# Optimization experiments

Hardware: AMD Instinct MI355X
Metric: run time of the kernel (lower is better)

Reference implementation:

```python
import jax, jax.numpy as jnp
from jax import lax
import numpy as np

K = 5  # length_inter_tile
EPS = 0.01


def _conv(x, w, b):
    y = lax.conv_general_dilated(x, w, (1, 1), ((1, 1), (1, 1)),
                                 dimension_numbers=('NCHW', 'OIHW', 'NCHW'))
    return y + b[None, :, None, None]


def _leaky(x):
    return jnp.where(x >= 0, x, 0.01 * x)


def _unfold(x, k=K):
    # torch F.unfold(x, k, padding=k//2): (b,c,h,w) -> (b, c*k*k, h*w), channel-major ordering
    b, c, h, w = x.shape
    p = k // 2
    xp = jnp.pad(x, ((0, 0), (0, 0), (p, p), (p, p)))
    pat = jnp.stack([xp[:, :, i:i + h, j:j + w] for i in range(k) for j in range(k)], axis=2)
    return pat.reshape(b, c * k * k, h * w)


def _fold(x, c, h, w, k=K):
    # torch F.fold: (b, c*k*k, h*w) -> (b, c, h, w) with overlap-add, padding=k//2
    b = x.shape[0]
    p = k // 2
    xr = x.reshape(b, c, k, k, h, w)
    out = jnp.zeros((b, c, h + 2 * p, w + 2 * p), x.dtype)
    for i in range(k):
        for j in range(k):
            out = out.at[:, :, i:i + h, j:j + w].add(xr[:, :, i, j])
    return out[:, :, p:p + h, p:p + w]


def _mmn(x, axes):
    mn = jnp.min(x, axis=axes, keepdims=True)
    mx = jnp.max(x, axis=axes, keepdims=True)
    return (x - mn) / (mx - mn + 0.001)


def setup_inputs() -> dict:
    key = jax.random.key(0)
    ks = jax.random.split(key, 8)
    b, t, ch_in, h, w = 1, 16, 10, 24, 24
    t_de, ch_de = 16, 12
    sc = 0.02
    return {
        'x': jax.random.normal(ks[0], (b, t, ch_in, h, w), jnp.float32),
        'design': jax.random.uniform(ks[1], (b, t_de, ch_de, h, w), jnp.float32),
        'gt': jax.random.uniform(ks[2], (b, t_de, 3, h, w), jnp.float32),
        'w1': jax.random.normal(ks[3], (1024, 160, 3, 3), jnp.float32) * sc,
        'b1': jnp.zeros((1024,), jnp.float32),
        'w2': jax.random.normal(ks[4], (1024, 1024, 3, 3), jnp.float32) * sc,
        'b2': jnp.zeros((1024,), jnp.float32),
        'w3': jax.random.normal(ks[5], (1024, 1024, 3, 3), jnp.float32) * sc,
        'b3': jnp.zeros((1024,), jnp.float32),
        'wf': jax.random.normal(ks[6], (6400, 1024, 3, 3), jnp.float32) * sc,
        'bf': jnp.zeros((6400,), jnp.float32),
    }


def _forward(x, design, gt, w1, b1, w2, b2, w3, b3, wf, bf):
    b, t, ch_in, h, w = x.shape
    t_de, ch_de = design.shape[1], design.shape[2]
    hw = h * w
    N = K * K  # num_inter

    # unfold design: (b, t_de*ch_de*N, hw) -> (b*hw, N, t_de, ch_de)
    d = _unfold(design.reshape(b, t_de * ch_de, h, w))
    d = d.transpose(0, 2, 1).reshape(b * hw, t_de * ch_de, N)
    d = d.transpose(0, 2, 1).reshape(b * hw, N, t_de, ch_de)

    # norm in each prediction window (per channel-group, per sample)
    d = jnp.concatenate([
        d[..., 0:1],
        _mmn(d[..., 1:4], (1, 2, 3)),
        _mmn(d[..., 4:5], (1, 2)),
        _mmn(d[..., 5:8], (1, 2, 3)),
        _mmn(d[..., 8:], (1, 2)),  # each grid channel independently
    ], axis=-1)

    M = b * hw * N
    domain = d.reshape(M, t_de, ch_de)
    X = d[:, :, :t, :].reshape(M, t, ch_de)

    # feature network (n_layers=4 -> 3 leaky convs) + weight head
    f = _leaky(_conv(x.reshape(b, t * ch_in, h, w), w1, b1))
    f = _leaky(_conv(f, w2, b2))
    f = _leaky(_conv(f, w3, b3))
    Wt = jnp.tanh(_conv(f, wf, bf))  # (b, N*t*t, h, w)
    Wm = Wt.reshape(b, N, t, t, h, w).transpose(0, 4, 5, 1, 2, 3).reshape(M, t, t)
    Wm = jnp.einsum('nij,nkj->nik', Wm, Wm) + jnp.eye(t, dtype=Wm.dtype)

    XTW = jnp.einsum('ntc,ntu->ncu', X, Wm)          # (M, ch_de, t)
    XTWX = jnp.einsum('nct,ntd->ncd', XTW, X)        # (M, ch_de, ch_de)
    A = XTWX.reshape(b * hw, N, ch_de, ch_de).sum(1) + EPS * jnp.eye(ch_de, dtype=XTWX.dtype)

    # reference for loss (unfolded)
    ref = _unfold(gt.reshape(b, t_de * 3, h, w))
    ref = ref.transpose(0, 2, 1).reshape(b * hw, t_de * 3, N)
    ref = ref.transpose(0, 2, 1).reshape(M, t_de, 3)

    outs, folded = [], []
    for ch in range(3):
        Y = _unfold(x[:, :, ch])                      # (b, t*N, hw)
        Y = Y.transpose(0, 2, 1).reshape(b * hw, t, N)
        Y = Y.transpose(0, 2, 1).reshape(M, t, 1)
        XTWY = jnp.einsum('nct,nto->nco', XTW, Y)
        Bv = XTWY.reshape(b * hw, N, ch_de, 1).sum(1)
        para = jnp.linalg.solve(A, Bv)                # (b*hw, ch_de, 1)
        para_r = jnp.broadcast_to(para[:, None], (b * hw, N, ch_de, 1)).reshape(M, ch_de, 1)
        o = jnp.einsum('ntc,nco->nto', domain, para_r)  # (M, t_de, 1)
        outs.append(o[..., 0])
        # overlap-add fold of per-window predictions
        oc = o.reshape(b, hw, N, t_de).transpose(0, 3, 2, 1).reshape(b, t_de * N, hw)
        num = _fold(oc, t_de, h, w)
        den = _fold(jnp.ones_like(oc), t_de, h, w)
        folded.append(num / den)

    out_for_loss = jnp.stack(outs, axis=-1)           # (M, t_de, 3)
    out = jnp.stack(folded, axis=2)                   # (b, t_de, 3, h, w)
    loss = jnp.mean(jnp.abs(out_for_loss - ref))      # L1 stand-in for loss_for_stit_v1
    return out, loss


def reference(x, design, gt, w1, b1, w2, b2, w3, b3, wf, bf):
    return _forward(x, design, gt, w1, b1, w2, b2, w3, b3, wf, bf)
```

## Files before the change

### kernel.cpp

```cpp
#include <hip/hip_runtime.h>
#include <math.h>


typedef __attribute__((ext_vector_type(8))) short sh8;
typedef __attribute__((ext_vector_type(4))) float f32x4;

#define OFF_PART 0UL
#define OFF_X2T  58982400UL
#define OFF_WTT  58982400UL
#define OFF_ACT  80216064UL
#define OFF_OB   82575360UL
#define OFF_LP   85340160UL


__device__ inline void glds16(const void* gsrc, void* ldst) {
    __builtin_amdgcn_global_load_lds((const __attribute__((address_space(1))) void*)gsrc,
                                     (__attribute__((address_space(3))) void*)ldst, 16, 0, 0);
}

__global__ __launch_bounds__(256) void im2col_kernel(const float* __restrict__ act,
                                                     char* __restrict__ x2t, int nrows) {
    int row = blockIdx.x * 256 + threadIdx.x;
    if (row >= nrows) return;
    int kc = row / 576, px = row % 576;
    int y = px / 24, x = px % 24;
    int k0 = kc * 32;
    int ic = k0 / 9;
    int tap = k0 - ic * 9;
    sh8 hv[4], lv[4];
#pragma unroll
    for (int e = 0; e < 32; ++e) {
        int dy = tap / 3, dx = tap - dy * 3;
        int yy = y + dy - 1, xx = x + dx - 1;
        float v = (yy >= 0 && yy < 24 && xx >= 0 && xx < 24)
                      ? act[ic * 576 + yy * 24 + xx] : 0.0f;
        unsigned u = __builtin_bit_cast(unsigned, v);
        hv[e / 8][e % 8] = (short)(u >> 16);
        float fh = __builtin_bit_cast(float, u & 0xFFFF0000u);
        lv[e / 8][e % 8] = (short)(__builtin_bit_cast(unsigned, v - fh) >> 16);
        if (++tap == 9) { tap = 0; ++ic; }
    }
    int pg = px >> 4, l15 = px & 15;
    char* dst = x2t + (long)kc * 73728 + pg * 2048 + l15 * 16;
#pragma unroll
    for (int q = 0; q < 4; ++q) {
        *(sh8*)(dst + q * 256) = hv[q];
        *(sh8*)(dst + 1024 + q * 256) = lv[q];
    }
}

__global__ void finalize_kernel(const float* __restrict__ part,
                                const float* __restrict__ bias,
                                float* __restrict__ act, int total, int nsplit) {
    int idx = blockIdx.x * 256 + threadIdx.x;
    if (idx >= total) return;
    float s = 0.0f;
    for (int k = 0; k < nsplit; k++) s += part[(long)k * total + idx];
    s += bias[idx / 576];
    act[idx] = s >= 0.0f ? s : 0.01f * s;
}

template<int SWZ>
__global__ __launch_bounds__(256, 4)
void conv_mfma8_kernel(const char* __restrict__ x2t,
                       const float* __restrict__ wgt,
                       float* __restrict__ part,
                       int K, int cps, int cout) {
    __shared__ __align__(1024) char sB[18432];
    __shared__ __align__(1024) char sA[16384];

    const int tid = threadIdx.x;
    const int lane = tid & 63;
    const int w = tid >> 6;
    const int q = lane >> 4, ln15 = lane & 15;
    const int lane16 = lane * 16;

    int ocb, pxq, s;
    if (SWZ) {
        int g = blockIdx.x;
        int p = (g & 7) * 100 + (g >> 3);
        ocb = p / 16;
        int rem = p % 16;
        s = rem >> 2; pxq = rem & 3;
    } else {
        ocb = blockIdx.x; pxq = blockIdx.y; s = blockIdx.z;
    }
    const int c0 = s * cps;

    const int st_oc = tid >> 1, st_h = tid & 1;
    const float* wrow = wgt + (long)(ocb * 128 + st_oc) * K + st_h * 16;
    const int wslot0 = (((st_h * 2 + 0) + (st_oc >> 1)) & 3) << 4;
    const int wslot1 = (((st_h * 2 + 1) + (st_oc >> 1)) & 3) << 4;

    int aoff[2];
#pragma unroll
    for (int ot = 0; ot < 2; ++ot) {
        int oc = w * 32 + ot * 16 + ln15;
        aoff[ot] = oc * 64 + (((q + (oc >> 1)) & 3) << 4);
    }

    f32x4 acc[2][9];
#pragma unroll
    for (int a = 0; a < 2; ++a)
#pragma unroll
        for (int j = 0; j < 9; ++j) acc[a][j] = f32x4{0.f, 0.f, 0.f, 0.f};

#pragma unroll 1
    for (int t = 0; t < cps; ++t) {
        const int cc = c0 + t;
        __syncthreads();
        const char* bsrc = x2t + (long)cc * 73728 + pxq * 18432;
        for (int u = w; u < 18; u += 4)
            glds16(bsrc + u * 1024 + lane16, sB + u * 1024);
        {
            const float* p = wrow + (long)cc * 32;
            float4 a0 = *(const float4*)(p);
            float4 a1 = *(const float4*)(p + 4);
            float4 a2 = *(const float4*)(p + 8);
            float4 a3 = *(const float4*)(p + 12);
            float av[16] = {a0.x, a0.y, a0.z, a0.w, a1.x, a1.y, a1.z, a1.w,
                            a2.x, a2.y, a2.z, a2.w, a3.x, a3.y, a3.z, a3.w};
            sh8 h8[2], l8[2];
#pragma unroll
            for (int e = 0; e < 16; ++e) {
                unsigned u = __builtin_bit_cast(unsigned, av[e]);
                h8[e / 8][e % 8] = (short)(u >> 16);
                float fh = __builtin_bit_cast(float, u & 0xFFFF0000u);
                l8[e / 8][e % 8] = (short)(__builtin_bit_cast(unsigned, av[e] - fh) >> 16);
            }
            char* hb = sA + st_oc * 64;
            *(sh8*)(hb + wslot0) = h8[0];
            *(sh8*)(hb + wslot1) = h8[1];
            *(sh8*)(hb + 8192 + wslot0) = l8[0];
            *(sh8*)(hb + 8192 + wslot1) = l8[1];
        }
        asm volatile("s_waitcnt vmcnt(0)" ::: "memory");
        __syncthreads();

        sh8 ah[2], al[2];
#pragma unroll
        for (int ot = 0; ot < 2; ++ot) {
            ah[ot] = *(const sh8*)(sA + aoff[ot]);
            al[ot] = *(const sh8*)(sA + 8192 + aoff[ot]);
        }
#pragma unroll
        for (int j = 0; j < 9; ++j) {
            sh8 bh = *(const sh8*)(sB + j * 2048 + lane16);
            sh8 bl = *(const sh8*)(sB + j * 2048 + 1024 + lane16);
#pragma unroll
            for (int ot = 0; ot < 2; ++ot) {
                acc[ot][j] = __builtin_amdgcn_mfma_f32_16x16x32_bf16(ah[ot], bh, acc[ot][j], 0, 0, 0);
                acc[ot][j] = __builtin_amdgcn_mfma_f32_16x16x32_bf16(al[ot], bh, acc[ot][j], 0, 0, 0);
                acc[ot][j] = __builtin_amdgcn_mfma_f32_16x16x32_bf16(ah[ot], bl, acc[ot][j], 0, 0, 0);
            }
        }
    }
#pragma unroll
    for (int ot = 0; ot < 2; ++ot) {
        int oc0 = ocb * 128 + w * 32 + ot * 16 + q * 4;
#pragma unroll
        for (int j = 0; j < 9; ++j) {
            int px = pxq * 144 + j * 16 + ln15;
#pragma unroll
            for (int vr = 0; vr < 4; ++vr)
                part[((long)s * cout + oc0 + vr) * 576 + px] = acc[ot][j][vr];
        }
    }
}

__global__ __launch_bounds__(256) void tanh_tr_kernel(const float* __restrict__ part,
                                                      const float* __restrict__ bias,
                                                      float* __restrict__ wtT, int nsplit) {
    __shared__ float tile[64][65];
    int oc0 = blockIdx.x * 64, p0 = blockIdx.y * 64;
    int tx = threadIdx.x, ty = threadIdx.y;
#pragma unroll
    for (int k = 0; k < 16; k++) {
        int row = ty + k * 4;
        float s = 0.f;
        for (int sp = 0; sp < nsplit; ++sp)
            s += part[((long)sp * 6400 + oc0 + row) * 576 + p0 + tx];
        tile[row][tx] = tanhf(s + bias[oc0 + row]);
    }
    __syncthreads();
#pragma unroll
    for (int k = 0; k < 16; k++) {
        int rr = ty + k * 4;
        wtT[(long)(p0 + rr) * 6400 + oc0 + tx] = tile[tx][rr];
    }
}

__global__ __launch_bounds__(256) void stagec_kernel(const float* __restrict__ design,
                                                     const float* __restrict__ wtT,
                                                     const float* __restrict__ xin,
                                                     const float* __restrict__ gt,
                                                     float* __restrict__ ob,
                                                     float* __restrict__ lp) {
    int p = blockIdx.x;
    int py = p / 24, px = p % 24;
    int tid = threadIdx.x;
    int lane = tid & 63, wv = tid >> 6;
    __shared__ float sX[4800];
    __shared__ float sW[6400];
    __shared__ float sY[1200];
    __shared__ float sP[192];
    __shared__ float sXTW[192];
    __shared__ float sA[144];
    __shared__ float sB[36];
    __shared__ double dM[180];
    __shared__ float spara[36];
    __shared__ float sred[256];
    __shared__ float sMnW[28], sMxW[28], sMn[7], sMx[7];

    for (int e = tid; e < 4800; e += 256) {
        int n = e / 192, r = e % 192, td = r / 12, cd = r % 12;
        int yy = py + n / 5 - 2, xx = px + n % 5 - 2;
        sX[e] = (yy >= 0 && yy < 24 && xx >= 0 && xx < 24)
                    ? design[(td * 12 + cd) * 576 + yy * 24 + xx] : 0.0f;
    }
    for (int e = tid; e < 6400; e += 256) sW[e] = wtT[(long)p * 6400 + e];
    for (int e = tid; e < 1200; e += 256) {
        int n = e / 48, t = (e % 48) / 3, ch = e % 3;
        int yy = py + n / 5 - 2, xx = px + n % 5 - 2;
        sY[e] = (yy >= 0 && yy < 24 && xx >= 0 && xx < 24)
                    ? xin[(t * 10 + ch) * 576 + yy * 24 + xx] : 0.0f;
    }
    if (tid < 144) sA[tid] = 0.0f;
    if (tid < 36) sB[tid] = 0.0f;
    __syncthreads();

    {
        float mn[7], mx[7];
#pragma unroll
        for (int g = 0; g < 7; g++) { mn[g] = 1e30f; mx[g] = -1e30f; }
        for (int e = tid; e < 4800; e += 256) {
            int cd = e % 12;
            if (cd >= 1) {
                int g = (cd <= 3) ? 0 : (cd == 4) ? 1 : (cd <= 7) ? 2 : 3 + (cd - 8);
                float v = sX[e];
                mn[g] = fminf(mn[g], v);
                mx[g] = fmaxf(mx[g], v);
            }
        }
#pragma unroll
        for (int s2 = 32; s2 >= 1; s2 >>= 1)
#pragma unroll
            for (int g = 0; g < 7; g++) {
                mn[g] = fminf(mn[g], __shfl_xor(mn[g], s2));
                mx[g] = fmaxf(mx[g], __shfl_xor(mx[g], s2));
            }
        if (lane == 0)
#pragma unroll
            for (int g = 0; g < 7; g++) { sMnW[wv * 7 + g] = mn[g]; sMxW[wv * 7 + g] = mx[g]; }
    }
    __syncthreads();
    if (tid < 7) {
        float a = fminf(fminf(sMnW[tid], sMnW[7 + tid]), fminf(sMnW[14 + tid], sMnW[21 + tid]));
        float b = fmaxf(fmaxf(sMxW[tid], sMxW[7 + tid]), fmaxf(sMxW[14 + tid], sMxW[21 + tid]));
        sMn[tid] = a; sMx[tid] = b;
    }
    __syncthreads();
    for (int e = tid; e < 4800; e += 256) {
        int cd = e % 12;
        if (cd >= 1) {
            int g = (cd <= 3) ? 0 : (cd == 4) ? 1 : (cd <= 7) ? 2 : 3 + (cd - 8);
            sX[e] = (sX[e] - sMn[g]) / (sMx[g] - sMn[g] + 0.001f);
        }
    }
    __syncthreads();

    for (int n = 0; n < 25; n++) {
        const float* X = sX + n * 192;
        const float* W = sW + n * 256;
        if (tid < 192) {
            int c = tid >> 4, j = tid & 15;
            float s = 0.0f;
#pragma unroll
            for (int t = 0; t < 16; t++) s = fmaf(X[t * 12 + c], W[t * 16 + j], s);
            sP[tid] = s;
        }
        __syncthreads();
        if (tid < 192) {
            int c = tid >> 4, u = tid & 15;
            float s = X[u * 12 + c];
#pragma unroll
            for (int j = 0; j < 16; j++) s = fmaf(sP[c * 16 + j], W[u * 16 + j], s);
            sXTW[tid] = s;
        }
        __syncthreads();
        if (tid < 144) {
            int c = tid / 12, d2 = tid % 12;
            float s = 0.0f;
#pragma unroll
            for (int t = 0; t < 16; t++) s = fmaf(sXTW[c * 16 + t], X[t * 12 + d2], s);
            sA[tid] += s;
        } else if (tid < 180) {
            int e = tid - 144;
            int c = e / 3, ch = e % 3;
            float s = 0.0f;
#pragma unroll
            for (int t = 0; t < 16; t++) s = fmaf(sXTW[c * 16 + t], sY[n * 48 + t * 3 + ch], s);
            sB[e] += s;
        }
        __syncthreads();
    }

    if (tid < 144) dM[(tid / 12) * 15 + (tid % 12)] = (double)sA[tid] + ((tid % 13 == 0) ? 0.01 : 0.0);
    if (tid < 36) dM[(tid / 3) * 15 + 12 + (tid % 3)] = (double)sB[tid];
    __syncthreads();
    {
        int rr = (tid < 180) ? tid / 15 : 11;
        int c2 = (tid < 180) ? tid % 15 : 14;
#pragma unroll 1
        for (int k = 0; k < 12; ++k) {
            double pinv = 1.0 / dM[k * 15 + k];
            double fkc = dM[k * 15 + c2] * pinv;
            double frk = dM[rr * 15 + k];
            double cur = dM[rr * 15 + c2];
            __syncthreads();
            if (tid < 180) dM[rr * 15 + c2] = (rr == k) ? fkc : fma(-frk, fkc, cur);
            __syncthreads();
        }
    }
    if (tid < 36) spara[tid] = (float)dM[(tid / 3) * 15 + 12 + (tid % 3)];
    __syncthreads();

    float lsum = 0.0f;
    for (int e = tid; e < 1200; e += 256) {
        int n = e / 48, td = (e % 48) / 3, ch = e % 3;
        float s = 0.0f;
#pragma unroll
        for (int c = 0; c < 12; c++) s = fmaf(sX[n * 192 + td * 12 + c], spara[c * 3 + ch], s);
        ob[((long)(p * 25 + n)) * 48 + td * 3 + ch] = s;
        int yy = py + n / 5 - 2, xx = px + n % 5 - 2;
        float rv = (yy >= 0 && yy < 24 && xx >= 0 && xx < 24)
                       ? gt[(td * 3 + ch) * 576 + yy * 24 + xx] : 0.0f;
        lsum += fabsf(s - rv);
    }
    sred[tid] = lsum;
    __syncthreads();
    for (int s = 128; s >= 1; s >>= 1) {
        if (tid < s) sred[tid] += sred[tid + s];
        __syncthreads();
    }
    if (tid == 0) lp[p] = sred[0];
}

__global__ void fold_kernel(const float* __restrict__ ob, float* __restrict__ out) {
    int idx = blockIdx.x * 256 + threadIdx.x;
    if (idx >= 27648) return;
    int td = idx / 1728;
    int rem = idx % 1728;
    int ch = rem / 576;
    int p = rem % 576;
    int y = p / 24, x = p % 24;
    float num = 0.0f;
    int den = 0;
    for (int i = 0; i < 5; i++) {
        int yy = y + 2 - i;
        if (yy < 0 || yy >= 24) continue;
        for (int j = 0; j < 5; j++) {
            int xx = x + 2 - j;
            if (xx < 0 || xx >= 24) continue;
            num += ob[((long)((yy * 24 + xx) * 25 + i * 5 + j)) * 48 + td * 3 + ch];
            den++;
        }
    }
    out[idx] = num / (float)den;
}

__global__ __launch_bounds__(64) void loss_kernel(const float* __restrict__ lp,
                                                  float* __restrict__ out) {
    int t = threadIdx.x;
    float s = 0.0f;
    for (int e = t; e < 576; e += 64) s += lp[e];
#pragma unroll
    for (int d = 32; d >= 1; d >>= 1) s += __shfl_xor(s, d);
    if (t == 0) out[27648] = s / 691200.0f;
}

extern "C" void kernel_launch(void* const* d_in, const int* in_sizes, int n_in,
                              void* d_out, int out_size, void* d_ws, size_t ws_size,
                              hipStream_t stream) {
    const float* x      = (const float*)d_in[0];
    const float* design = (const float*)d_in[1];
    const float* gt     = (const float*)d_in[2];
    const float* w1     = (const float*)d_in[3];
    const float* b1     = (const float*)d_in[4];
    const float* w2     = (const float*)d_in[5];
    const float* b2     = (const float*)d_in[6];
    const float* w3     = (const float*)d_in[7];
    const float* b3     = (const float*)d_in[8];
    const float* wf     = (const float*)d_in[9];
    const float* bf     = (const float*)d_in[10];
    float* out = (float*)d_out;
    char* wsb  = (char*)d_ws;

    float* part = (float*)(wsb + OFF_PART);
    char*  x2t  = wsb + OFF_X2T;
    float* wtT  = (float*)(wsb + OFF_WTT);
    float* act  = (float*)(wsb + OFF_ACT);
    float* ob   = (float*)(wsb + OFF_OB);
    float* lp   = (float*)(wsb + OFF_LP);

    im2col_kernel<<<102, 256, 0, stream>>>(x, x2t, 45 * 576);
    conv_mfma8_kernel<0><<<dim3(8, 4, 15), 256, 0, stream>>>(x2t, w1, part, 1440, 3, 1024);
    finalize_kernel<<<2304, 256, 0, stream>>>(part, b1, act, 589824, 15);
    im2col_kernel<<<648, 256, 0, stream>>>(act, x2t, 288 * 576);
    conv_mfma8_kernel<0><<<dim3(8, 4, 16), 256, 0, stream>>>(x2t, w2, part, 9216, 18, 1024);
    finalize_kernel<<<2304, 256, 0, stream>>>(part, b2, act, 589824, 16);
    im2col_kernel<<<648, 256, 0, stream>>>(act, x2t, 288 * 576);
    conv_mfma8_kernel<0><<<dim3(8, 4, 16), 256, 0, stream>>>(x2t, w3, part, 9216, 18, 1024);
    finalize_kernel<<<2304, 256, 0, stream>>>(part, b3, act, 589824, 16);
    im2col_kernel<<<648, 256, 0, stream>>>(act, x2t, 288 * 576);
    conv_mfma8_kernel<1><<<800, 256, 0, stream>>>(x2t, wf, part, 9216, 72, 6400);
    tanh_tr_kernel<<<dim3(100, 9), dim3(64, 4), 0, stream>>>(part, bf, wtT, 4);

    stagec_kernel<<<576, 256, 0, stream>>>(design, wtT, x, gt, ob, lp);
    fold_kernel<<<108, 256, 0, stream>>>(ob, out);
    loss_kernel<<<1, 64, 0, stream>>>(lp, out);
}
```

Measured before the change: 506.6 us.

## Replace LDS-staged conv GEMM with register double-buffered direct loads

The conv MFMA kernel no longer stages A and B tiles through shared memory with barriers. Each wave now loads its B fragments and weight rows straight from global memory into registers and prefetches the next K-chunk while the MFMAs for the current one run. The final conv layer drops from 4 to 2 split-K partitions (400 blocks), which shrinks the partial-sum buffer, and the workspace offsets move to match. The trade-off is higher register pressure (launch bounds go from 4 to 2 blocks per CU), redundant global loads of B across waves that LDS used to share, and less parallelism in the final layer.

```diff
diff --git a/kernel.cpp b/kernel.cpp
--- a/kernel.cpp
+++ b/kernel.cpp
@@ -6,17 +6,12 @@
 typedef __attribute__((ext_vector_type(4))) float f32x4;
 
 #define OFF_PART 0UL
-#define OFF_X2T  58982400UL
-#define OFF_WTT  58982400UL
-#define OFF_ACT  80216064UL
-#define OFF_OB   82575360UL
-#define OFF_LP   85340160UL
-
-
-__device__ inline void glds16(const void* gsrc, void* ldst) {
-    __builtin_amdgcn_global_load_lds((const __attribute__((address_space(1))) void*)gsrc,
-                                     (__attribute__((address_space(3))) void*)ldst, 16, 0, 0);
-}
+#define OFF_X2T  37748736UL
+#define OFF_WTT  37748736UL
+#define OFF_ACT  58982400UL
+#define OFF_OB   61341696UL
+#define OFF_LP   64106496UL
+
 
 __global__ __launch_bounds__(256) void im2col_kernel(const float* __restrict__ act,
                                                      char* __restrict__ x2t, int nrows) {
@@ -60,15 +55,23 @@
     act[idx] = s >= 0.0f ? s : 0.01f * s;
 }
 
+__device__ inline void cvt_split8(const float4& a0, const float4& a1, sh8& h8, sh8& l8) {
+    float av[8] = {a0.x, a0.y, a0.z, a0.w, a1.x, a1.y, a1.z, a1.w};
+#pragma unroll
+    for (int e = 0; e < 8; ++e) {
+        unsigned u = __builtin_bit_cast(unsigned, av[e]);
+        h8[e] = (short)(u >> 16);
+        float fh = __builtin_bit_cast(float, u & 0xFFFF0000u);
+        l8[e] = (short)(__builtin_bit_cast(unsigned, av[e] - fh) >> 16);
+    }
+}
+
 template<int SWZ>
-__global__ __launch_bounds__(256, 4)
-void conv_mfma8_kernel(const char* __restrict__ x2t,
+__global__ __launch_bounds__(256, 2)
+void conv_mfma9_kernel(const char* __restrict__ x2t,
                        const float* __restrict__ wgt,
                        float* __restrict__ part,
                        int K, int cps, int cout) {
-    __shared__ __align__(1024) char sB[18432];
-    __shared__ __align__(1024) char sA[16384];
-
     const int tid = threadIdx.x;
     const int lane = tid & 63;
     const int w = tid >> 6;
@@ -78,81 +81,75 @@
     int ocb, pxq, s;
     if (SWZ) {
         int g = blockIdx.x;
-        int p = (g & 7) * 100 + (g >> 3);
-        ocb = p / 16;
-        int rem = p % 16;
+        int p = (g & 7) * 50 + (g >> 3);
+        ocb = p >> 3;
+        int rem = p & 7;
         s = rem >> 2; pxq = rem & 3;
     } else {
         ocb = blockIdx.x; pxq = blockIdx.y; s = blockIdx.z;
     }
     const int c0 = s * cps;
 
-    const int st_oc = tid >> 1, st_h = tid & 1;
-    const float* wrow = wgt + (long)(ocb * 128 + st_oc) * K + st_h * 16;
-    const int wslot0 = (((st_h * 2 + 0) + (st_oc >> 1)) & 3) << 4;
-    const int wslot1 = (((st_h * 2 + 1) + (st_oc >> 1)) & 3) << 4;
-
-    int aoff[2];
-#pragma unroll
-    for (int ot = 0; ot < 2; ++ot) {
-        int oc = w * 32 + ot * 16 + ln15;
-        aoff[ot] = oc * 64 + (((q + (oc >> 1)) & 3) << 4);
-    }
+    const float* arow0 = wgt + (long)(ocb * 128 + w * 32 + ln15) * K + q * 8;
+    const float* arow1 = arow0 + (long)16 * K;
+    const char* bbase = x2t + (long)pxq * 18432;
 
     f32x4 acc[2][9];
 #pragma unroll
     for (int a = 0; a < 2; ++a)
 #pragma unroll
         for (int j = 0; j < 9; ++j) acc[a][j] = f32x4{0.f, 0.f, 0.f, 0.f};
+
+    sh8 bh[9], bl[9];
+    {
+        const char* bc = bbase + (long)c0 * 73728;
+#pragma unroll
+        for (int j = 0; j < 9; ++j) {
+            bh[j] = *(const sh8*)(bc + j * 2048 + lane16);
+            bl[j] = *(const sh8*)(bc + j * 2048 + 1024 + lane16);
+        }
+    }
+    sh8 ah[2], al[2];
+    float4 an[4];
+    {
+        const float* p0 = arow0 + (long)c0 * 32;
+        const float* p1 = arow1 + (long)c0 * 32;
+        float4 t0 = *(const float4*)(p0), t1 = *(const float4*)(p0 + 4);
+        float4 t2 = *(const float4*)(p1), t3 = *(const float4*)(p1 + 4);
+        cvt_split8(t0, t1, ah[0], al[0]);
+        cvt_split8(t2, t3, ah[1], al[1]);
+        const int c1 = (cps > 1) ? c0 + 1 : c0;
+        const float* n0 = arow0 + (long)c1 * 32;
+        const float* n1 = arow1 + (long)c1 * 32;
+        an[0] = *(const float4*)(n0); an[1] = *(const float4*)(n0 + 4);
+        an[2] = *(const float4*)(n1); an[3] = *(const float4*)(n1 + 4);
+    }
 
 #pragma unroll 1
     for (int t = 0; t < cps; ++t) {
-        const int cc = c0 + t;
-        __syncthreads();
-        const char* bsrc = x2t + (long)cc * 73728 + pxq * 18432;
-        for (int u = w; u < 18; u += 4)
-            glds16(bsrc + u * 1024 + lane16, sB + u * 1024);
-        {
-            const float* p = wrow + (long)cc * 32;
-            float4 a0 = *(const float4*)(p);
-            float4 a1 = *(const float4*)(p + 4);
-            float4 a2 = *(const float4*)(p + 8);
-            float4 a3 = *(const float4*)(p + 12);
-            float av[16] = {a0.x, a0.y, a0.z, a0.w, a1.x, a1.y, a1.z, a1.w,
-                            a2.x, a2.y, a2.z, a2.w, a3.x, a3.y, a3.z, a3.w};
-            sh8 h8[2], l8[2];
-#pragma unroll
-            for (int e = 0; e < 16; ++e) {
-                unsigned u = __builtin_bit_cast(unsigned, av[e]);
-                h8[e / 8][e % 8] = (short)(u >> 16);
-                float fh = __builtin_bit_cast(float, u & 0xFFFF0000u);
-                l8[e / 8][e % 8] = (short)(__builtin_bit_cast(unsigned, av[e] - fh) >> 16);
-            }
-            char* hb = sA + st_oc * 64;
-            *(sh8*)(hb + wslot0) = h8[0];
-            *(sh8*)(hb + wslot1) = h8[1];
-            *(sh8*)(hb + 8192 + wslot0) = l8[0];
-            *(sh8*)(hb + 8192 + wslot1) = l8[1];
-        }
-        asm volatile("s_waitcnt vmcnt(0)" ::: "memory");
-        __syncthreads();
-
-        sh8 ah[2], al[2];
-#pragma unroll
-        for (int ot = 0; ot < 2; ++ot) {
-            ah[ot] = *(const sh8*)(sA + aoff[ot]);
-            al[ot] = *(const sh8*)(sA + 8192 + aoff[ot]);
-        }
+        const int cn = (t + 1 < cps) ? (c0 + t + 1) : (c0 + cps - 1);
+        const char* bnext = bbase + (long)cn * 73728;
 #pragma unroll
         for (int j = 0; j < 9; ++j) {
-            sh8 bh = *(const sh8*)(sB + j * 2048 + lane16);
-            sh8 bl = *(const sh8*)(sB + j * 2048 + 1024 + lane16);
-#pragma unroll
-            for (int ot = 0; ot < 2; ++ot) {
-                acc[ot][j] = __builtin_amdgcn_mfma_f32_16x16x32_bf16(ah[ot], bh, acc[ot][j], 0, 0, 0);
-                acc[ot][j] = __builtin_amdgcn_mfma_f32_16x16x32_bf16(al[ot], bh, acc[ot][j], 0, 0, 0);
-                acc[ot][j] = __builtin_amdgcn_mfma_f32_16x16x32_bf16(ah[ot], bl, acc[ot][j], 0, 0, 0);
-            }
+            sh8 bhj = bh[j];
+            sh8 blj = bl[j];
+            acc[0][j] = __builtin_amdgcn_mfma_f32_16x16x32_bf16(ah[0], bhj, acc[0][j], 0, 0, 0);
+            acc[1][j] = __builtin_amdgcn_mfma_f32_16x16x32_bf16(ah[1], bhj, acc[1][j], 0, 0, 0);
+            acc[0][j] = __builtin_amdgcn_mfma_f32_16x16x32_bf16(al[0], bhj, acc[0][j], 0, 0, 0);
+            acc[1][j] = __builtin_amdgcn_mfma_f32_16x16x32_bf16(al[1], bhj, acc[1][j], 0, 0, 0);
+            acc[0][j] = __builtin_amdgcn_mfma_f32_16x16x32_bf16(ah[0], blj, acc[0][j], 0, 0, 0);
+            acc[1][j] = __builtin_amdgcn_mfma_f32_16x16x32_bf16(ah[1], blj, acc[1][j], 0, 0, 0);
+            bh[j] = *(const sh8*)(bnext + j * 2048 + lane16);
+            bl[j] = *(const sh8*)(bnext + j * 2048 + 1024 + lane16);
+        }
+        if (t + 1 < cps) {
+            cvt_split8(an[0], an[1], ah[0], al[0]);
+            cvt_split8(an[2], an[3], ah[1], al[1]);
+            const int c2 = (t + 2 < cps) ? (c0 + t + 2) : (c0 + cps - 1);
+            const float* n0 = arow0 + (long)c2 * 32;
+            const float* n1 = arow1 + (long)c2 * 32;
+            an[0] = *(const float4*)(n0); an[1] = *(const float4*)(n0 + 4);
+            an[2] = *(const float4*)(n1); an[3] = *(const float4*)(n1 + 4);
         }
     }
 #pragma unroll
@@ -255,9 +252,8 @@
     }
     __syncthreads();
     if (tid < 7) {
-        float a = fminf(fminf(sMnW[tid], sMnW[7 + tid]), fminf(sMnW[14 + tid], sMnW[21 + tid]));
-        float b = fmaxf(fmaxf(sMxW[tid], sMxW[7 + tid]), fmaxf(sMxW[14 + tid], sMxW[21 + tid]));
-        sMn[tid] = a; sMx[tid] = b;
+        sMn[tid] = fminf(fminf(sMnW[tid], sMnW[7 + tid]), fminf(sMnW[14 + tid], sMnW[21 + tid]));
+        sMx[tid] = fmaxf(fmaxf(sMxW[tid], sMxW[7 + tid]), fmaxf(sMxW[14 + tid], sMxW[21 + tid]));
     }
     __syncthreads();
     for (int e = tid; e < 4800; e += 256) {
@@ -404,17 +400,17 @@
     float* lp   = (float*)(wsb + OFF_LP);
 
     im2col_kernel<<<102, 256, 0, stream>>>(x, x2t, 45 * 576);
-    conv_mfma8_kernel<0><<<dim3(8, 4, 15), 256, 0, stream>>>(x2t, w1, part, 1440, 3, 1024);
+    conv_mfma9_kernel<0><<<dim3(8, 4, 15), 256, 0, stream>>>(x2t, w1, part, 1440, 3, 1024);
     finalize_kernel<<<2304, 256, 0, stream>>>(part, b1, act, 589824, 15);
     im2col_kernel<<<648, 256, 0, stream>>>(act, x2t, 288 * 576);
-    conv_mfma8_kernel<0><<<dim3(8, 4, 16), 256, 0, stream>>>(x2t, w2, part, 9216, 18, 1024);
+    conv_mfma9_kernel<0><<<dim3(8, 4, 16), 256, 0, stream>>>(x2t, w2, part, 9216, 18, 1024);
     finalize_kernel<<<2304, 256, 0, stream>>>(part, b2, act, 589824, 16);
     im2col_kernel<<<648, 256, 0, stream>>>(act, x2t, 288 * 576);
-    conv_mfma8_kernel<0><<<dim3(8, 4, 16), 256, 0, stream>>>(x2t, w3, part, 9216, 18, 1024);
+    conv_mfma9_kernel<0><<<dim3(8, 4, 16), 256, 0, stream>>>(x2t, w3, part, 9216, 18, 1024);
     finalize_kernel<<<2304, 256, 0, stream>>>(part, b3, act, 589824, 16);
     im2col_kernel<<<648, 256, 0, stream>>>(act, x2t, 288 * 576);
-    conv_mfma8_kernel<1><<<800, 256, 0, stream>>>(x2t, wf, part, 9216, 72, 6400);
-    tanh_tr_kernel<<<dim3(100, 9), dim3(64, 4), 0, stream>>>(part, bf, wtT, 4);
+    conv_mfma9_kernel<1><<<400, 256, 0, stream>>>(x2t, wf, part, 9216, 144, 6400);
+    tanh_tr_kernel<<<dim3(100, 9), dim3(64, 4), 0, stream>>>(part, bf, wtT, 2);
 
     stagec_kernel<<<576, 256, 0, stream>>>(design, wtT, x, gt, ob, lp);
     fold_kernel<<<108, 256, 0, stream>>>(ob, out);
```

Measured after the change: 731.4 us. +44.4%, slower.

## Add larger-tile final conv kernel with direct global-to-LDS weight loads

Applied to the files above, without the earlier changes.

Adds a dedicated kernel for the large final convolution (6400 output channels). Each block computes 128 output channels by 288 pixels, with waves split into 2x2 over channels and pixels, which doubles per-block reuse of the loaded weight and activation tiles and halves the grid to 400 blocks. Weights are streamed into LDS with async global_load_lds using an XOR swizzle, and the fp32 to bf16 hi/lo split happens at fragment read time. The cost is higher register and LDS use (occupancy bound set to 2), and each chunk is fully loaded and waited on before compute, with no double buffering.

```diff
diff --git a/kernel.cpp b/kernel.cpp
--- a/kernel.cpp
+++ b/kernel.cpp
@@ -60,7 +60,6 @@
     act[idx] = s >= 0.0f ? s : 0.01f * s;
 }
 
-template<int SWZ>
 __global__ __launch_bounds__(256, 4)
 void conv_mfma8_kernel(const char* __restrict__ x2t,
                        const float* __restrict__ wgt,
@@ -75,16 +74,7 @@
     const int q = lane >> 4, ln15 = lane & 15;
     const int lane16 = lane * 16;
 
-    int ocb, pxq, s;
-    if (SWZ) {
-        int g = blockIdx.x;
-        int p = (g & 7) * 100 + (g >> 3);
-        ocb = p / 16;
-        int rem = p % 16;
-        s = rem >> 2; pxq = rem & 3;
-    } else {
-        ocb = blockIdx.x; pxq = blockIdx.y; s = blockIdx.z;
-    }
+    const int ocb = blockIdx.x, pxq = blockIdx.y, s = blockIdx.z;
     const int c0 = s * cps;
 
     const int st_oc = tid >> 1, st_h = tid & 1;
@@ -161,6 +151,99 @@
 #pragma unroll
         for (int j = 0; j < 9; ++j) {
             int px = pxq * 144 + j * 16 + ln15;
+#pragma unroll
+            for (int vr = 0; vr < 4; ++vr)
+                part[((long)s * cout + oc0 + vr) * 576 + px] = acc[ot][j][vr];
+        }
+    }
+}
+
+__global__ __launch_bounds__(256, 2)
+void conv_mfmaF_kernel(const char* __restrict__ x2t,
+                       const float* __restrict__ wgt,
+                       float* __restrict__ part,
+                       int K, int cps, int cout) {
+    __shared__ __align__(1024) char sA[16384];
+    __shared__ __align__(1024) char sB[36864];
+
+    const int tid = threadIdx.x;
+    const int lane = tid & 63;
+    const int w = tid >> 6;
+    const int wo = w >> 1, wp = w & 1;
+    const int q = lane >> 4, ln15 = lane & 15;
+    const int lane16 = lane * 16;
+
+    int g = blockIdx.x;
+    int p = (g & 7) * 50 + (g >> 3);
+    const int pxh = p & 1;
+    const int s = (p >> 1) & 3;
+    const int ocb = p >> 3;
+    const long K4 = (long)K * 4;
+    const int c0 = s * cps;
+
+    const int arow = lane >> 3;
+    const int acol = (lane & 7) * 16;
+    const int sw = (ln15 & 7) << 4;
+
+    f32x4 acc[4][9];
+#pragma unroll
+    for (int a = 0; a < 4; ++a)
+#pragma unroll
+        for (int j = 0; j < 9; ++j) acc[a][j] = f32x4{0.f, 0.f, 0.f, 0.f};
+
+    const char* wsrc0 = (const char*)wgt + (long)(ocb * 128) * K4;
+
+#pragma unroll 1
+    for (int t = 0; t < cps; ++t) {
+        const int cc = c0 + t;
+        __syncthreads();
+        {
+            const char* wsrc = wsrc0 + (long)cc * 128;
+            for (int it = w; it < 16; it += 4) {
+                int r = it * 8 + arow;
+                glds16(wsrc + (long)r * K4 + (acol ^ ((r & 7) << 4)), sA + it * 1024);
+            }
+            const char* bsrc = x2t + (long)cc * 73728 + pxh * 36864;
+            for (int u = w; u < 36; u += 4)
+                glds16(bsrc + u * 1024 + lane16, sB + u * 1024);
+        }
+        asm volatile("s_waitcnt vmcnt(0)" ::: "memory");
+        __syncthreads();
+
+        sh8 ah[4], al[4];
+#pragma unroll
+        for (int ot = 0; ot < 4; ++ot) {
+            const char* ap = sA + (wo * 64 + ot * 16 + ln15) * 128;
+            float4 a0 = *(const float4*)(ap + ((q * 32) ^ sw));
+            float4 a1 = *(const float4*)(ap + ((q * 32 + 16) ^ sw));
+            float av[8] = {a0.x, a0.y, a0.z, a0.w, a1.x, a1.y, a1.z, a1.w};
+#pragma unroll
+            for (int e = 0; e < 8; ++e) {
+                unsigned u = __builtin_bit_cast(unsigned, av[e]);
+                ah[ot][e] = (short)(u >> 16);
+                float fh = __builtin_bit_cast(float, u & 0xFFFF0000u);
+                al[ot][e] = (short)(__builtin_bit_cast(unsigned, av[e] - fh) >> 16);
+            }
+        }
+#pragma unroll
+        for (int j = 0; j < 9; ++j) {
+            const char* bp = sB + (wp * 9 + j) * 2048 + lane16;
+            sh8 bh = *(const sh8*)(bp);
+            sh8 bl = *(const sh8*)(bp + 1024);
+#pragma unroll
+            for (int ot = 0; ot < 4; ++ot) {
+                acc[ot][j] = __builtin_amdgcn_mfma_f32_16x16x32_bf16(ah[ot], bh, acc[ot][j], 0, 0, 0);
+                acc[ot][j] = __builtin_amdgcn_mfma_f32_16x16x32_bf16(al[ot], bh, acc[ot][j], 0, 0, 0);
+                acc[ot][j] = __builtin_amdgcn_mfma_f32_16x16x32_bf16(ah[ot], bl, acc[ot][j], 0, 0, 0);
+            }
+        }
+    }
+#pragma unroll
+    for (int ot = 0; ot < 4; ++ot) {
+        int oc0 = ocb * 128 + wo * 64 + ot * 16 + q * 4;
+#pragma unroll
+        for (int j = 0; j < 9; ++j) {
+            int px = pxh * 288 + wp * 144 + j * 16 + ln15;
 #pragma unroll
             for (int vr = 0; vr < 4; ++vr)
                 part[((long)s * cout + oc0 + vr) * 576 + px] = acc[ot][j][vr];
@@ -255,9 +338,8 @@
     }
     __syncthreads();
     if (tid < 7) {
-        float a = fminf(fminf(sMnW[tid], sMnW[7 + tid]), fminf(sMnW[14 + tid], sMnW[21 + tid]));
-        float b = fmaxf(fmaxf(sMxW[tid], sMxW[7 + tid]), fmaxf(sMxW[14 + tid], sMxW[21 + tid]));
-        sMn[tid] = a; sMx[tid] = b;
+        sMn[tid] = fminf(fminf(sMnW[tid], sMnW[7 + tid]), fminf(sMnW[14 + tid], sMnW[21 + tid]));
+        sMx[tid] = fmaxf(fmaxf(sMxW[tid], sMxW[7 + tid]), fmaxf(sMxW[14 + tid], sMxW[21 + tid]));
     }
     __syncthreads();
     for (int e = tid; e < 4800; e += 256) {
@@ -404,16 +486,16 @@
     float* lp   = (float*)(wsb + OFF_LP);
 
     im2col_kernel<<<102, 256, 0, stream>>>(x, x2t, 45 * 576);
-    conv_mfma8_kernel<0><<<dim3(8, 4, 15), 256, 0, stream>>>(x2t, w1, part, 1440, 3, 1024);
+    conv_mfma8_kernel<<<dim3(8, 4, 15), 256, 0, stream>>>(x2t, w1, part, 1440, 3, 1024);
     finalize_kernel<<<2304, 256, 0, stream>>>(part, b1, act, 589824, 15);
     im2col_kernel<<<648, 256, 0, stream>>>(act, x2t, 288 * 576);
-    conv_mfma8_kernel<0><<<dim3(8, 4, 16), 256, 0, stream>>>(x2t, w2, part, 9216, 18, 1024);
+    conv_mfma8_kernel<<<dim3(8, 4, 16), 256, 0, stream>>>(x2t, w2, part, 9216, 18, 1024);
     finalize_kernel<<<2304, 256, 0, stream>>>(part, b2, act, 589824, 16);
     im2col_kernel<<<648, 256, 0, stream>>>(act, x2t, 288 * 576);
-    conv_mfma8_kernel<0><<<dim3(8, 4, 16), 256, 0, stream>>>(x2t, w3, part, 9216, 18, 1024);
+    conv_mfma8_kernel<<<dim3(8, 4, 16), 256, 0, stream>>>(x2t, w3, part, 9216, 18, 1024);
     finalize_kernel<<<2304, 256, 0, stream>>>(part, b3, act, 589824, 16);
     im2col_kernel<<<648, 256, 0, stream>>>(act, x2t, 288 * 576);
-    conv_mfma8_kernel<1><<<800, 256, 0, stream>>>(x2t, wf, part, 9216, 72, 6400);
+    conv_mfmaF_kernel<<<400, 256, 0, stream>>>(x2t, wf, part, 9216, 72, 6400);
     tanh_tr_kernel<<<dim3(100, 9), dim3(64, 4), 0, stream>>>(part, bf, wtT, 4);
 
     stagec_kernel<<<576, 256, 0, stream>>>(design, wtT, x, gt, ob, lp);
```

Measured after the change: 468.3 us (median of 2 runs). -7.6%, faster.
